# Kernel tuning notes

Measured on AMD Instinct MI355X. Metric: run time of the kernel, lower is better.

The kernel has to match this reference:

```python
import jax, jax.numpy as jnp
import numpy as np

B, C, H = 2, 32, 64  # batch, base channel, bottleneck spatial size
EPS = 1e-5


def _conv(x, w, b, pad):
    # standard NCHW conv, stride 1
    out = jax.lax.conv_general_dilated(x, w, (1, 1), [(pad, pad), (pad, pad)],
                                       dimension_numbers=("NCHW", "OIHW", "NCHW"))
    return out + b[None, :, None, None]


def _inorm(x):
    # InstanceNorm2d, affine=False (torch default)
    m = jnp.mean(x, axis=(2, 3), keepdims=True)
    v = jnp.var(x, axis=(2, 3), keepdims=True)
    return (x - m) * jax.lax.rsqrt(v + EPS)


def _patches3(x):
    # x: (B,C,H,W) -> (B,C,9,H-2,W-2); 3x3 patches, stride 1, VALID
    oh, ow = x.shape[-2] - 2, x.shape[-1] - 2
    return jnp.stack([x[:, :, i:i + oh, j:j + ow] for i in range(3) for j in range(3)], axis=2)


def _pac_kernel(g):
    # gaussian pixel-adaptive kernel (NVlabs/pac, kernel_type='gaussian', normalize_kernel=False)
    # g: (B,Cg,H,W) -> K: (B,9,H,W), K = exp(-0.5*||f_nbr - f_center||^2)
    gp = jnp.pad(g, ((0, 0), (0, 0), (1, 1), (1, 1)))
    p = _patches3(gp)                      # (B,Cg,9,H,W)
    d = p - g[:, :, None]                  # center is offset (1,1) == g itself
    return jnp.exp(-0.5 * jnp.sum(d * d, axis=1))


def _pacconvT(x, g, w, b):
    # PacConvTranspose2d: kernel_size=3, stride=2, padding=1, output_padding=1
    # native impl: zero-upsample, pad (k-1)-p=1 left/top and 1+out_pad=2 right/bottom,
    # then pixel-adaptive conv with weight.permute(1,0,2,3) (no spatial flip, per PAC).
    Bc, Cin, Hh, Ww = x.shape
    z = jnp.zeros((Bc, Cin, 2 * Hh - 1, 2 * Ww - 1), x.dtype).at[:, :, ::2, ::2].set(x)
    z = jnp.pad(z, ((0, 0), (0, 0), (1, 2), (1, 2)))
    p = _patches3(z)                       # (B,Cin,9,2H,2W)
    k = _pac_kernel(g)                     # (B,9,2H,2W)
    wf = jnp.transpose(w, (1, 0, 2, 3)).reshape(w.shape[1], w.shape[0], 9)  # (Cout,Cin,9)
    out = jnp.einsum('bckhw,bkhw,ock->bohw', p, k, wf)
    return out + b[None, :, None, None]


def _w(key, shape, scale):
    return jax.random.normal(key, shape, dtype=jnp.float32) * scale


def setup_inputs():
    key = jax.random.key(0)
    ks = jax.random.split(key, 20)
    return {
        "x": jax.random.normal(ks[0], (B, 8 * C, H, H), jnp.float32),
        "ef_lv2": jax.random.normal(ks[1], (B, 2 * C, 2 * H, 2 * H), jnp.float32),
        "ef_lv1": jax.random.normal(ks[2], (B, C, 4 * H, 4 * H), jnp.float32),
        "W_down": _w(ks[3], (4 * C, 8 * C, 3, 3), (8 * C * 9) ** -0.5),
        "b_down": _w(ks[4], (4 * C,), 0.01),
        "W_mid": _w(ks[5], (4 * C, 4 * C, 1, 1), (4 * C) ** -0.5),
        "b_mid": _w(ks[6], (4 * C,), 0.01),
        "W_adj2": _w(ks[7], (4 * C, 2 * C, 3, 3), 0.002),  # small: keeps gaussian kernel non-degenerate
        "b_adj2": _w(ks[8], (4 * C,), 0.01),
        "W_adj1": _w(ks[9], (2 * C, C, 3, 3), 0.004),
        "b_adj1": _w(ks[10], (2 * C,), 0.01),
        "W16": _w(ks[11], (4 * C, 2 * C, 3, 3), (4 * C * 9) ** -0.5),  # convT layout (Cin,Cout,kh,kw)
        "b16": _w(ks[12], (2 * C,), 0.01),
        "W20": _w(ks[13], (2 * C, C, 3, 3), (2 * C * 9) ** -0.5),
        "b20": _w(ks[14], (C,), 0.01),
        "W24": _w(ks[15], (3, C, 3, 3), (C * 9) ** -0.5),
        "b24": _w(ks[16], (3,), 0.01),
    }


def reference(x, ef_lv2, ef_lv1, W_down, b_down, W_mid, b_mid, W_adj2, b_adj2,
              W_adj1, b_adj1, W16, b16, W20, b20, W24, b24):
    x = _conv(_inorm(x), W_down, b_down, 1)          # layer13: norm + channel-down 8C->4C
    x = _conv(x, W_mid, b_mid, 0) + x                # middle_layer13 1x1 + residual
    g2 = _conv(ef_lv2, W_adj2, b_adj2, 1)            # adjust_ef_lv2 2C->4C
    x = _pacconvT(x, g2, W16, b16)                   # layer16: 4C->2C, x2 spatial
    x = _inorm(x) + x                                # layer17 + residual (twice)
    x = _inorm(x) + x
    g1 = _conv(ef_lv1, W_adj1, b_adj1, 1)            # adjust_ef_lv1 C->2C
    x = _pacconvT(x, g1, W20, b20)                   # layer20: 2C->C, x2 spatial
    x = _inorm(x) + x                                # layer21 + residual (twice)
    x = _inorm(x) + x
    return _conv(x, W24, b24, 1)                     # layer24: C->3
```

## Files before the change

### kernel.cpp

```cpp
#include <hip/hip_runtime.h>

#define EPS 1e-5f

typedef short sh8 __attribute__((ext_vector_type(8)));
typedef float f32x4 __attribute__((ext_vector_type(4)));

__device__ __forceinline__ ushort f2b(float f) {
    unsigned u = __float_as_uint(f);
    u += 0x7fffu + ((u >> 16) & 1u);
    return (ushort)(u >> 16);
}

__device__ __forceinline__ void istat_body(int ch, const float* __restrict__ in,
                                           float* st, int HW)
{
    __shared__ double sh[512];
    const float* p = in + (size_t)ch * HW;
    double s = 0.0, s2 = 0.0;
    for (int i = threadIdx.x * 4; i < HW; i += 1024) {
        float4 v = *(const float4*)(p + i);
        s  += (double)v.x + (double)v.y + (double)v.z + (double)v.w;
        s2 += (double)v.x * v.x + (double)v.y * v.y
            + (double)v.z * v.z + (double)v.w * v.w;
    }
    sh[threadIdx.x] = s; sh[256 + threadIdx.x] = s2;
    __syncthreads();
    for (int o = 128; o > 0; o >>= 1) {
        if ((int)threadIdx.x < o) {
            sh[threadIdx.x]       += sh[threadIdx.x + o];
            sh[256 + threadIdx.x] += sh[256 + threadIdx.x + o];
        }
        __syncthreads();
    }
    if (threadIdx.x == 0) {
        double m = sh[0] / (double)HW;
        double v = sh[256] / (double)HW - m * m;
        st[2 * ch]     = (float)m;
        st[2 * ch + 1] = (float)(v < 0.0 ? 0.0 : v);
    }
}

__device__ __forceinline__ void ipad_body(int bxi, int b,
    const float* __restrict__ in, const float* __restrict__ st,
    ushort* __restrict__ ob, int C, int H, int W, int pad, int n4)
{
    int idx = bxi * 256 + threadIdx.x;
    if (idx >= n4) return;
    int cpp = C >> 2;
    int pp = idx / cpp, c0 = (idx - pp * cpp) * 4;
    int Wp = W + 2 * pad, Hp = H + 2 * pad;
    int yp = pp / Wp, xp = pp - yp * Wp;
    int y = yp - pad, x = xp - pad;
    ushort4 o;
    if (y >= 0 && y < H && x >= 0 && x < W) {
        size_t HW = (size_t)H * W;
        const float* ib = in + (size_t)b * C * HW + (size_t)y * W + x;
        #pragma unroll
        for (int u = 0; u < 4; u++) {
            int chg = b * C + c0 + u;
            float m = st[2 * chg];
            float inv = rsqrtf(st[2 * chg + 1] + EPS);
            float v = ib[(size_t)(c0 + u) * HW];
            ((ushort*)&o)[u] = f2b((v - m) * inv);
        }
    } else { o.x = o.y = o.z = o.w = 0; }
    *(ushort4*)(ob + ((size_t)b * Hp * Wp + pp) * C + c0) = o;
}

__device__ __forceinline__ void pad_body(int bxi, int b,
    const float* __restrict__ in, ushort* __restrict__ ob,
    int C, int H, int W, int pad, int n4)
{
    int idx = bxi * 256 + threadIdx.x;
    if (idx >= n4) return;
    int cpp = C >> 2;
    int pp = idx / cpp, c0 = (idx - pp * cpp) * 4;
    int Wp = W + 2 * pad, Hp = H + 2 * pad;
    int yp = pp / Wp, xp = pp - yp * Wp;
    int y = yp - pad, x = xp - pad;
    ushort4 o;
    if (y >= 0 && y < H && x >= 0 && x < W) {
        const float* ib = in + ((size_t)b * C) * H * W + (size_t)y * W + x;
        size_t HW = (size_t)H * W;
        o.x = f2b(ib[(size_t)(c0    ) * HW]);
        o.y = f2b(ib[(size_t)(c0 + 1) * HW]);
        o.z = f2b(ib[(size_t)(c0 + 2) * HW]);
        o.w = f2b(ib[(size_t)(c0 + 3) * HW]);
    } else { o.x = o.y = o.z = o.w = 0; }
    *(ushort4*)(ob + ((size_t)b * Hp * Wp + pp) * C + c0) = o;
}

__device__ __forceinline__ void wprep_body(int bxi,
    const float* W16, const float* W20, const float* Wd, const float* Wa2,
    const float* Wa1,
    ushort* wT1b, ushort* wT2b, ushort* wbD, ushort* wbA2b, ushort* wbA1b)
{
    int idx = bxi * 256 + threadIdx.x;
    if (idx < 73728) {
        int to = idx / 128, ci = idx - to * 128;
        int t = to / 64, o = to - t * 64;
        wT1b[idx] = f2b(W16[((size_t)ci * 64 + o) * 9 + t]);
        return;
    } idx -= 73728;
    if (idx < 18432) {
        int to = idx / 64, ci = idx - to * 64;
        int t = to / 32, o = to - t * 32;
        wT2b[idx] = f2b(W20[((size_t)ci * 32 + o) * 9 + t]);
        return;
    } idx -= 18432;
    if (idx < 294912) {
        int co = idx / 2304, r = idx - co * 2304;
        int t = r / 256, ci = r - t * 256;
        wbD[idx] = f2b(Wd[((size_t)co * 256 + ci) * 9 + t]);
        return;
    } idx -= 294912;
    if (idx < 73728) {
        int co = idx / 576, r = idx - co * 576;
        int t = r / 64, ci = r - t * 64;
        wbA2b[idx] = f2b(Wa2[((size_t)co * 64 + ci) * 9 + t]);
        return;
    } idx -= 73728;
    if (idx < 18432) {
        int co = idx / 288, r = idx - co * 288;
        int t = r / 32, ci = r - t * 32;
        wbA1b[idx] = f2b(Wa1[((size_t)co * 32 + ci) * 9 + t]);
        return;
    }
}

template<int CI, int TAPS, int KCH, int CPB>
__device__ __forceinline__ void mg2f_body(int bx, int by, int bz,
    const ushort* __restrict__ inb, const ushort* __restrict__ wb,
    const float* __restrict__ bias, float* __restrict__ outp,
    int wshift, int Wp, int NS, size_t SS,
    size_t in_bstride, size_t out_bstride, int HW, ushort* bsm)
{
    constexpr int CPBSH = (CPB == 1) ? 0 : (CPB == 2) ? 1 : 2;
    constexpr int SPR   = TAPS * CPB;
    constexpr int TOT   = TAPS * KCH;
    constexpr int PS    = SPR * 32 + 8;

    int b = bz / NS, sl = bz - b * NS;
    int cilo = sl * (KCH * 32);
    int tid = threadIdx.x;
    int wv = tid >> 6, l = tid & 63;
    int lane16 = l & 15, quad = l >> 4;
    int klane = quad * 8;
    int pb = bx * 128 + wv * 32;
    int nb0 = by * 32;

    int base[2];
    #pragma unroll
    for (int i = 0; i < 2; i++) {
        int pm = pb + i * 16 + lane16;
        if (TAPS == 9) {
            int W = 1 << wshift;
            int y = pm >> wshift, xx = pm & (W - 1);
            base[i] = (y + 1) * Wp + (xx + 1);
        } else base[i] = pm;
    }
    int nn[2];
    nn[0] = nb0 + lane16; nn[1] = nb0 + 16 + lane16;

    const ushort* inbb = inb + (size_t)b * in_bstride + cilo + klane;
    const ushort* wbs  = wb + cilo;
    const ushort* bp0 = bsm + lane16 * PS + klane;
    const ushort* bp1 = bsm + (16 + lane16) * PS + klane;

    f32x4 vz = {0.f, 0.f, 0.f, 0.f};
    f32x4 acc[2][2] = {{vz, vz}, {vz, vz}};
    sh8 A[3][2];

    #define LDA(ss, av) { \
        int r_ = (ss) / SPR; int l_ = (ss) - r_ * SPR; \
        int t_ = l_ >> CPBSH; int ch_ = r_ * CPB + (l_ & (CPB - 1)); \
        int dof_ = 0; \
        if (TAPS == 9) { \
            int dy_ = (t_ * 43) >> 7; \
            int dx_ = t_ - dy_ * 3; \
            dof_ = (dy_ - 1) * Wp + (dx_ - 1); \
        } \
        av[0] = *(const sh8*)(inbb + (size_t)(base[0] + dof_) * CI + (ch_ << 5)); \
        av[1] = *(const sh8*)(inbb + (size_t)(base[1] + dof_) * CI + (ch_ << 5)); \
    }

    LDA(0, A[0])
    if (TOT > 1) LDA(1, A[1])

    #pragma unroll
    for (int r = 0; r < KCH / CPB; r++) {
        if (r) __syncthreads();
        {
            constexpr int elems = 32 * SPR * 4;
            for (int j = tid; j < elems; j += 256) {
                int n  = j / (SPR * 4);
                int rr = j - n * (SPR * 4);
                int kc = rr >> 2, c8 = rr & 3;
                int t_ = kc >> CPBSH, co = kc & (CPB - 1);
                int ch_ = r * CPB + co;
                sh8 v = *(const sh8*)(wbs
                    + ((size_t)(nb0 + n) * TAPS + t_) * CI + (ch_ << 5) + (c8 << 3));
                *(sh8*)(bsm + n * PS + (kc << 5) + (c8 << 3)) = v;
            }
        }
        __syncthreads();
        #pragma unroll
        for (int li = 0; li < SPR; li++) {
            const int s = r * SPR + li;
            if (s + 2 < TOT) LDA(s + 2, A[(s + 2) % 3])
            sh8 b0 = *(const sh8*)(bp0 + (li << 5));
            sh8 b1 = *(const sh8*)(bp1 + (li << 5));
            acc[0][0] = __builtin_amdgcn_mfma_f32_16x16x32_bf16(A[s % 3][0], b0, acc[0][0], 0, 0, 0);
            acc[0][1] = __builtin_amdgcn_mfma_f32_16x16x32_bf16(A[s % 3][0], b1, acc[0][1], 0, 0, 0);
            acc[1][0] = __builtin_amdgcn_mfma_f32_16x16x32_bf16(A[s % 3][1], b0, acc[1][0], 0, 0, 0);
            acc[1][1] = __builtin_amdgcn_mfma_f32_16x16x32_bf16(A[s % 3][1], b1, acc[1][1], 0, 0, 0);
        }
    }
    #undef LDA

    float* ob = outp + (size_t)sl * SS + (size_t)b * out_bstride;
    #pragma unroll
    for (int j = 0; j < 2; j++) {
        float bb = bias ? bias[nn[j]] : 0.f;
        #pragma unroll
        for (int i = 0; i < 2; i++) {
            int p0 = pb + i * 16 + quad * 4;
            *(float4*)(ob + (size_t)nn[j] * HW + p0) =
                make_float4(acc[i][j][0] + bb, acc[i][j][1] + bb,
                            acc[i][j][2] + bb, acc[i][j][3] + bb);
        }
    }
}

__device__ __forceinline__ void pack4_body(int bxi, int zy,
    const float* __restrict__ g, float* __restrict__ part,
    int Cg, int CS, int H, int W, int NS, size_t SS)
{
    int b = zy / NS, sl = zy - b * NS;
    int WC = W >> 2;
    int idx = bxi * 256 + threadIdx.x;
    int y = idx / WC, xc = idx - y * WC;
    int x0 = xc << 2;
    bool lz = (x0 == 0), rz = (x0 + 4 == W);
    float acc[9][4];
    #pragma unroll
    for (int t = 0; t < 9; t++)
        #pragma unroll
        for (int p = 0; p < 4; p++) acc[t][p] = 0.f;

    const float* gb = g + ((size_t)b * Cg + sl * CS) * H * W;
    for (int ci = 0; ci < CS; ci++) {
        const float* gc = gb + (size_t)ci * H * W;
        float e[3][6];
        #pragma unroll
        for (int r = 0; r < 3; r++) {
            int yy = y + r - 1;
            float4 v = make_float4(0.f, 0.f, 0.f, 0.f);
            if (yy >= 0 && yy < H)
                v = *(const float4*)(gc + (size_t)yy * W + x0);
            float lf = __shfl_up(v.w, 1);
            float rt = __shfl_down(v.x, 1);
            e[r][0] = lz ? 0.f : lf;
            e[r][1] = v.x; e[r][2] = v.y; e[r][3] = v.z; e[r][4] = v.w;
            e[r][5] = rz ? 0.f : rt;
        }
        #pragma unroll
        for (int i = 0; i < 3; i++)
            #pragma unroll
            for (int j = 0; j < 3; j++)
                #pragma unroll
                for (int p = 0; p < 4; p++) {
                    float d = e[i][p + j] - e[1][p + 1];
                    acc[i * 3 + j][p] = fmaf(d, d, acc[i * 3 + j][p]);
                }
    }
    size_t HW = (size_t)H * W;
    #pragma unroll
    for (int t = 0; t < 9; t++) {
        float4 o;
        if (NS == 1) {
            o = make_float4(expf(-0.5f * acc[t][0]), expf(-0.5f * acc[t][1]),
                            expf(-0.5f * acc[t][2]), expf(-0.5f * acc[t][3]));
        } else {
            o = make_float4(acc[t][0], acc[t][1], acc[t][2], acc[t][3]);
        }
        *(float4*)(part + (size_t)sl * SS + ((size_t)b * 9 + t) * HW
                   + (size_t)y * W + x0) = o;
    }
}

__device__ __forceinline__ void reduce_body(int bxi,
    const float* __restrict__ part, const float* __restrict__ bias,
    const float* res, float* out, int HW, int Co, int NS, size_t SS)
{
    int i4 = (bxi * 256 + threadIdx.x) * 4;
    float4 a = make_float4(0.f, 0.f, 0.f, 0.f);
    for (int s = 0; s < NS; s++) {
        float4 p = *(const float4*)(part + (size_t)s * SS + i4);
        a.x += p.x; a.y += p.y; a.z += p.z; a.w += p.w;
    }
    int c = (i4 / HW) % Co;
    float bb = bias[c];
    if (res) {
        float4 r = *(const float4*)(res + i4);
        a.x += r.x; a.y += r.y; a.z += r.z; a.w += r.w;
    }
    *(float4*)(out + i4) = make_float4(a.x + bb, a.y + bb, a.z + bb, a.w + bb);
}

__device__ __forceinline__ void expcomb_body(int bxi,
    const float* __restrict__ part, float* __restrict__ K, int NS, size_t SS)
{
    int i4 = (bxi * 256 + threadIdx.x) * 4;
    float4 a = make_float4(0.f, 0.f, 0.f, 0.f);
    for (int s = 0; s < NS; s++) {
        float4 p = *(const float4*)(part + (size_t)s * SS + i4);
        a.x += p.x; a.y += p.y; a.z += p.z; a.w += p.w;
    }
    *(float4*)(K + i4) = make_float4(expf(-0.5f * a.x), expf(-0.5f * a.y),
                                     expf(-0.5f * a.z), expf(-0.5f * a.w));
}

__global__ __launch_bounds__(256) void pro_k(
    const float* x, const float* ef2, const float* ef1,
    const float* W16, const float* W20, const float* Wd, const float* Wa2,
    const float* Wa1,
    ushort* wT1b, ushort* wT2b, ushort* wbD, ushort* wbA2b, ushort* wbA1b,
    float* st0, ushort* padA2b, ushort* padA1b)
{
    int bid = blockIdx.x;
    if (bid < 1872) {
        wprep_body(bid, W16, W20, Wd, Wa2, Wa1, wT1b, wT2b, wbD, wbA2b, wbA1b);
        return;
    } bid -= 1872;
    if (bid < 512) { istat_body(bid, x, st0, 4096); return; } bid -= 512;
    if (bid < 2114) {
        pad_body(bid % 1057, bid / 1057, ef2, padA2b, 64, 128, 128, 1, 270400);
        return;
    } bid -= 2114;
    pad_body(bid % 2081, bid / 2081, ef1, padA1b, 32, 256, 256, 1, 532512);
}

__global__ __launch_bounds__(256) void l1_k(
    const float* x, const float* st0, ushort* padDb,
    const ushort* padA2b, const ushort* wbA2b, const float* ba2, float* g2,
    const ushort* padA1b, const ushort* wbA1b, const float* ba1, float* g1)
{
    __shared__ ushort smem[32 * (9 * 32 + 8)];
    int bid = blockIdx.x;
    if (bid < 2178) {
        ipad_body(bid % 1089, bid / 1089, x, st0, padDb, 256, 64, 64, 1, 278784);
        return;
    } bid -= 2178;
    if (bid < 1024) {
        mg2f_body<64, 9, 2, 1>(bid & 127, (bid >> 7) & 3, bid >> 9,
            padA2b, wbA2b, ba2, g2, 7, 130, 1, (size_t)0,
            (size_t)1081600, (size_t)2097152, 16384, smem);
        return;
    } bid -= 1024;
    mg2f_body<32, 9, 1, 1>(bid & 511, (bid >> 9) & 1, bid >> 10,
        padA1b, wbA1b, ba1, g1, 8, 258, 1, (size_t)0,
        (size_t)2130048, (size_t)4194304, 65536, smem);
}

__global__ __launch_bounds__(256) void l2_k(
    const ushort* padDb, const ushort* wbD, float* Pd,
    const float* g1, float* PK1, const float* g2, float* PK2)
{
    __shared__ ushort smem[32 * (9 * 32 + 8)];
    int bid = blockIdx.x;
    if (bid < 512) {
        pack4_body(bid & 63, bid >> 6, g1, PK1, 64, 16, 256, 256, 4, (size_t)1179648);
        return;
    } bid -= 512;
    if (bid < 256) {
        pack4_body(bid & 15, bid >> 4, g2, PK2, 128, 16, 128, 128, 8, (size_t)294912);
        return;
    } bid -= 256;
    mg2f_body<256, 9, 1, 1>(bid & 31, (bid >> 5) & 3, bid >> 7,
        padDb, wbD, nullptr, Pd, 6, 66, 8, (size_t)1048576,
        (size_t)1115136, (size_t)524288, 4096, smem);
}

__global__ __launch_bounds__(256) void l3_k(
    const float* Pd, const float* bd, float* x1,
    const float* PK1, float* K1, const float* PK2, float* K2)
{
    int bid = blockIdx.x;
    if (bid < 1024) {
        reduce_body(bid, Pd, bd, nullptr, x1, 4096, 128, 8, (size_t)1048576);
        return;
    } bid -= 1024;
    if (bid < 1152) {
        expcomb_body(bid, PK1, K1, 4, (size_t)1179648);
        return;
    } bid -= 1152;
    expcomb_body(bid, PK2, K2, 8, (size_t)294912);
}

__global__ __launch_bounds__(256) void conv1x1f_k(
    const float* __restrict__ x1, const float* __restrict__ Wm,
    const float* __restrict__ bm, ushort* __restrict__ x2b)
{
    __shared__ float wsm[1024];
    int b = blockIdx.z;
    int co0 = blockIdx.y * 8;
    int tid = threadIdx.x;
    for (int j = tid; j < 1024; j += 256) {
        int co = j >> 7, ci = j & 127;
        wsm[j] = Wm[(size_t)(co0 + co) * 128 + ci];
    }
    __syncthreads();
    int px0 = (blockIdx.x * 256 + tid) * 4;
    const float* ib = x1 + (size_t)b * 524288 + px0;
    float acc[8][4];
    #pragma unroll
    for (int j = 0; j < 8; j++)
        #pragma unroll
        for (int p = 0; p < 4; p++) acc[j][p] = 0.f;
    for (int ci = 0; ci < 128; ci++) {
        float4 v = *(const float4*)(ib + (size_t)ci * 4096);
        #pragma unroll
        for (int j = 0; j < 8; j++) {
            float wv = wsm[j * 128 + ci];
            acc[j][0] = fmaf(v.x, wv, acc[j][0]);
            acc[j][1] = fmaf(v.y, wv, acc[j][1]);
            acc[j][2] = fmaf(v.z, wv, acc[j][2]);
            acc[j][3] = fmaf(v.w, wv, acc[j][3]);
        }
    }
    float vals[4][8];
    #pragma unroll
    for (int j = 0; j < 8; j++) {
        float4 r = *(const float4*)(ib + (size_t)(co0 + j) * 4096);
        float bb = bm[co0 + j];
        vals[0][j] = acc[j][0] + r.x + bb;
        vals[1][j] = acc[j][1] + r.y + bb;
        vals[2][j] = acc[j][2] + r.z + bb;
        vals[3][j] = acc[j][3] + r.w + bb;
    }
    #pragma unroll
    for (int p = 0; p < 4; p++) {
        sh8 ov;
        #pragma unroll
        for (int j = 0; j < 8; j++) ((ushort*)&ov)[j] = f2b(vals[p][j]);
        *(sh8*)(x2b + ((size_t)b * 4096 + px0 + p) * 128 + co0) = ov;
    }
}

__global__ __launch_bounds__(256) void istat1_k(const float* __restrict__ in,
                                                float* st, int HW)
{
    istat_body(blockIdx.x, in, st, HW);
}

template<int CI, int TAPS, int KCH, int CPB>
__global__ __launch_bounds__(256) void mg2f_k(
    const ushort* __restrict__ inb, const ushort* __restrict__ wb,
    const float* __restrict__ bias, float* __restrict__ outp,
    int wshift, int Wp, int NS, size_t SS,
    size_t in_bstride, size_t out_bstride, int HW)
{
    constexpr int PS = TAPS * CPB * 32 + 8;
    __shared__ ushort smem[32 * PS];
    mg2f_body<CI, TAPS, KCH, CPB>(blockIdx.x, blockIdx.y, blockIdx.z,
        inb, wb, bias, outp, wshift, Wp, NS, SS, in_bstride, out_bstride, HW, smem);
}

__global__ __launch_bounds__(256) void iapad_k(const float* __restrict__ in,
    const float* __restrict__ st, ushort* __restrict__ ob, int HW, int Co)
{
    int i4 = (blockIdx.x * 256 + threadIdx.x) * 4;
    int ch = i4 / HW;
    int p = i4 - ch * HW;
    int b = ch / Co, c = ch - b * Co;
    float m = st[2 * ch];
    float inv = rsqrtf(st[2 * ch + 1] + EPS);
    float4 v = *(const float4*)(in + i4);
    ushort* op = ob + ((size_t)b * HW + p) * Co + c;
    op[0]              = f2b(v.x + 2.f * (v.x - m) * inv);
    op[(size_t)Co]     = f2b(v.y + 2.f * (v.y - m) * inv);
    op[(size_t)Co * 2] = f2b(v.z + 2.f * (v.z - m) * inv);
    op[(size_t)Co * 3] = f2b(v.w + 2.f * (v.w - m) * inv);
}

template<int NCO>
__global__ __launch_bounds__(256) void conv3x3_d(const float* __restrict__ in,
    const float* __restrict__ w, const float* __restrict__ bias,
    float* __restrict__ outp, const float* __restrict__ st,
    int Ci, int CS, int H, int W, int Co, int NS, size_t SS)
{
    int z = blockIdx.z;
    int b = z / NS, sl = z - b * NS;
    int WC = W >> 2;
    int idx = blockIdx.x * 256 + threadIdx.x;
    int xc = idx % WC, y = idx / WC;
    int x0 = xc << 2;
    bool lz = (x0 == 0), rz = (x0 + 4 == W);
    int co0 = blockIdx.y * NCO;
    float acc[NCO][4];
    #pragma unroll
    for (int j = 0; j < NCO; j++)
        #pragma unroll
        for (int p = 0; p < 4; p++) acc[j][p] = 0.f;

    const float* ib = in + ((size_t)b * Ci + sl * CS) * H * W;
    for (int ci = 0; ci < CS; ci++) {
        const float* ic = ib + (size_t)ci * H * W;
        int cig = sl * CS + ci;
        float sa = 1.f, sb = 0.f;
        if (st) {
            int chg = b * Ci + cig;
            float m = st[2 * chg];
            float inv = rsqrtf(st[2 * chg + 1] + EPS);
            sa = 1.f + 2.f * inv;
            sb = -2.f * m * inv;
        }
        float e[3][6];
        #pragma unroll
        for (int r = 0; r < 3; r++) {
            int yy = y + r - 1;
            float4 v = make_float4(0.f, 0.f, 0.f, 0.f);
            if (yy >= 0 && yy < H) {
                v = *(const float4*)(ic + (size_t)yy * W + x0);
                if (st) {
                    v.x = fmaf(v.x, sa, sb); v.y = fmaf(v.y, sa, sb);
                    v.z = fmaf(v.z, sa, sb); v.w = fmaf(v.w, sa, sb);
                }
            }
            float lf = __shfl_up(v.w, 1);
            float rt = __shfl_down(v.x, 1);
            e[r][0] = lz ? 0.f : lf;
            e[r][1] = v.x; e[r][2] = v.y; e[r][3] = v.z; e[r][4] = v.w;
            e[r][5] = rz ? 0.f : rt;
        }
        #pragma unroll
        for (int j = 0; j < NCO; j++) {
            const float* wj = w + ((size_t)(co0 + j) * Ci + cig) * 9;
            #pragma unroll
            for (int r = 0; r < 3; r++) {
                float w0 = wj[3 * r], w1 = wj[3 * r + 1], w2 = wj[3 * r + 2];
                #pragma unroll
                for (int p = 0; p < 4; p++)
                    acc[j][p] = fmaf(e[r][p], w0,
                                fmaf(e[r][p + 1], w1,
                                fmaf(e[r][p + 2], w2, acc[j][p])));
            }
        }
    }
    size_t HW = (size_t)H * W;
    #pragma unroll
    for (int j = 0; j < NCO; j++) {
        float bb = bias ? bias[co0 + j] : 0.f;
        float4 o = make_float4(acc[j][0] + bb, acc[j][1] + bb,
                               acc[j][2] + bb, acc[j][3] + bb);
        float* op = outp + (size_t)sl * SS
                  + ((size_t)b * Co + co0 + j) * HW + (size_t)y * W + x0;
        *(float4*)op = o;
    }
}

__global__ __launch_bounds__(256) void reduce_k(const float* __restrict__ part,
    const float* __restrict__ bias, const float* res, float* out,
    int HW, int Co, int NS, size_t SS)
{
    reduce_body(blockIdx.x, part, bias, res, out, HW, Co, NS, SS);
}

template<int NCO>
__global__ __launch_bounds__(256) void pacsc_k(const float* __restrict__ Gin,
    const float* __restrict__ K, const float* __restrict__ bias,
    float* __restrict__ out, int Cout, int Hi, int Wi, size_t gstride)
{
    int b = blockIdx.z;
    int H = Hi << 1, W = Wi << 1;
    int HW = H * W, HWi = Hi * Wi, WC = W >> 2;
    int idx = blockIdx.x * 256 + threadIdx.x;
    int half = (H >> 1) * WC;
    int py = (idx >= half) ? 1 : 0;
    int r = idx - py * half;
    int ry = r / WC;
    int y = 2 * ry + py;
    int x0 = (r - ry * WC) << 2;
    int yi = y >> 1, xi0 = x0 >> 1;
    int co0 = blockIdx.y * NCO;
    const float* G  = Gin + (size_t)b * gstride;
    const float* Kb = K + (size_t)b * 9 * HW;
    float* ob = out + (size_t)b * Cout * HW;
    size_t krow = (size_t)y * W + x0;
    bool vok = (xi0 + 2 < Wi);

    if (py == 0) {
        float k4a = Kb[(size_t)4 * HW + krow],     k4b = Kb[(size_t)4 * HW + krow + 2];
        float k3a = Kb[(size_t)3 * HW + krow + 1], k3b = Kb[(size_t)3 * HW + krow + 3];
        float k5a = Kb[(size_t)5 * HW + krow + 1], k5b = Kb[(size_t)5 * HW + krow + 3];
        #pragma unroll
        for (int j = 0; j < NCO; j++) {
            int co = co0 + j;
            size_t rowb = (size_t)yi * Wi + xi0;
            const float* g3 = G + (size_t)(3 * Cout + co) * HWi + rowb;
            const float* g4 = G + (size_t)(4 * Cout + co) * HWi + rowb;
            const float* g5 = G + (size_t)(5 * Cout + co) * HWi + rowb;
            float bb = bias[co];
            float g5b = vok ? g5[2] : 0.f;
            float o0 = fmaf(k4a, g4[0], bb);
            float o1 = fmaf(k3a, g3[0], fmaf(k5a, g5[1], bb));
            float o2 = fmaf(k4b, g4[1], bb);
            float o3 = fmaf(k3b, g3[1], fmaf(k5b, g5b, bb));
            *(float4*)(ob + (size_t)co * HW + krow) = make_float4(o0, o1, o2, o3);
        }
    } else {
        bool yok = (yi + 1 < Hi);
        float k1a = Kb[(size_t)1 * HW + krow],     k1b = Kb[(size_t)1 * HW + krow + 2];
        float k7a = Kb[(size_t)7 * HW + krow],     k7b = Kb[(size_t)7 * HW + krow + 2];
        float k0a = Kb[(size_t)0 * HW + krow + 1], k0b = Kb[(size_t)0 * HW + krow + 3];
        float k2a = Kb[(size_t)2 * HW + krow + 1], k2b = Kb[(size_t)2 * HW + krow + 3];
        float k6a = Kb[(size_t)6 * HW + krow + 1], k6b = Kb[(size_t)6 * HW + krow + 3];
        float k8a = Kb[(size_t)8 * HW + krow + 1], k8b = Kb[(size_t)8 * HW + krow + 3];
        #pragma unroll
        for (int j = 0; j < NCO; j++) {
            int co = co0 + j;
            size_t row0 = (size_t)yi * Wi + xi0;
            size_t row1 = (size_t)(yi + 1) * Wi + xi0;
            const float* g0 = G + (size_t)(0 * Cout + co) * HWi + row0;
            const float* g1 = G + (size_t)(1 * Cout + co) * HWi + row0;
            const float* g2 = G + (size_t)(2 * Cout + co) * HWi + row0;
            const float* g6 = G + (size_t)(6 * Cout + co) * HWi + row1;
            const float* g7 = G + (size_t)(7 * Cout + co) * HWi + row1;
            const float* g8 = G + (size_t)(8 * Cout + co) * HWi + row1;
            float bb = bias[co];
            float g2b = vok ? g2[2] : 0.f;
            float g6a = yok ? g6[0] : 0.f, g6b = yok ? g6[1] : 0.f;
            float g7a = yok ? g7[0] : 0.f, g7b = yok ? g7[1] : 0.f;
            float g8a = yok ? g8[1] : 0.f;
            float g8b = (yok && vok) ? g8[2] : 0.f;
            float o0 = fmaf(k1a, g1[0], fmaf(k7a, g7a, bb));
            float o1 = fmaf(k0a, g0[0], fmaf(k2a, g2[1],
                       fmaf(k6a, g6a, fmaf(k8a, g8a, bb))));
            float o2 = fmaf(k1b, g1[1], fmaf(k7b, g7b, bb));
            float o3 = fmaf(k0b, g0[1], fmaf(k2b, g2b,
                       fmaf(k6b, g6b, fmaf(k8b, g8b, bb))));
            *(float4*)(ob + (size_t)co * HW + krow) = make_float4(o0, o1, o2, o3);
        }
    }
}

extern "C" void kernel_launch(void* const* d_in, const int* in_sizes, int n_in,
                              void* d_out, int out_size, void* d_ws, size_t ws_size,
                              hipStream_t stream)
{
    const float* x   = (const float*)d_in[0];
    const float* ef2 = (const float*)d_in[1];
    const float* ef1 = (const float*)d_in[2];
    const float* Wd  = (const float*)d_in[3];
    const float* bd  = (const float*)d_in[4];
    const float* Wm  = (const float*)d_in[5];
    const float* bm  = (const float*)d_in[6];
    const float* Wa2 = (const float*)d_in[7];
    const float* ba2 = (const float*)d_in[8];
    const float* Wa1 = (const float*)d_in[9];
    const float* ba1 = (const float*)d_in[10];
    const float* W16 = (const float*)d_in[11];
    const float* b16 = (const float*)d_in[12];
    const float* W20 = (const float*)d_in[13];
    const float* b20 = (const float*)d_in[14];
    const float* W24 = (const float*)d_in[15];
    const float* b24 = (const float*)d_in[16];
    float* out = (float*)d_out;

    float* P = (float*)d_ws;
    size_t o = 0;
    auto take = [&](size_t n) { float* p = P + o; o += n; return p; };
    ushort* padDb  = (ushort*)take(1115136);
    ushort* wbD    = (ushort*)take(147456);
    float*  Pd     = take(8388608);
    float*  x1     = take(1048576);
    ushort* x2b    = (ushort*)take(524288);
    ushort* padA2b = (ushort*)take(1081600);
    ushort* wbA2b  = (ushort*)take(36864);
    float*  g2     = take(4194304);
    float*  PK2    = take(2359296);
    float*  K2     = take(294912);
    float*  Gin1   = take(4718592);
    float*  x3     = take(2097152);
    ushort* x3b    = (ushort*)take(1048576);
    ushort* padA1b = (ushort*)take(2130048);
    ushort* wbA1b  = (ushort*)take(9216);
    float*  g1     = take(8388608);
    float*  PK1    = take(4718592);
    float*  K1     = take(1179648);
    float*  Gin2   = take(9437184);
    float*  x5     = take(4194304);
    float*  Pf     = take(1572864);
    ushort* wT1b   = (ushort*)take(36864);
    ushort* wT2b   = (ushort*)take(9216);
    float*  ST     = take(1408);
    float* st0 = ST; float* st3 = ST + 1024; float* st5 = ST + 1280;

    pro_k<<<dim3(8660), dim3(256), 0, stream>>>(
        x, ef2, ef1, W16, W20, Wd, Wa2, Wa1,
        wT1b, wT2b, wbD, wbA2b, wbA1b, st0, padA2b, padA1b);

    l1_k<<<dim3(5250), dim3(256), 0, stream>>>(
        x, st0, padDb, padA2b, wbA2b, ba2, g2, padA1b, wbA1b, ba1, g1);

    l2_k<<<dim3(2816), dim3(256), 0, stream>>>(
        padDb, wbD, Pd, g1, PK1, g2, PK2);

    l3_k<<<dim3(2464), dim3(256), 0, stream>>>(Pd, bd, x1, PK1, K1, PK2, K2);

    conv1x1f_k<<<dim3(4, 16, 2), dim3(256), 0, stream>>>(x1, Wm, bm, x2b);

    mg2f_k<128, 1, 4, 4><<<dim3(32, 18, 2), dim3(256), 0, stream>>>(
        x2b, wT1b, nullptr, Gin1, 0, 0, 1, (size_t)0,
        (size_t)524288, (size_t)2359296, 4096);
    pacsc_k<2><<<dim3(16, 32, 2), dim3(256), 0, stream>>>(
        Gin1, K2, b16, x3, 64, 64, 64, (size_t)2359296);

    istat1_k<<<dim3(128), dim3(256), 0, stream>>>(x3, st3, 16384);
    iapad_k<<<dim3(2048), dim3(256), 0, stream>>>(x3, st3, x3b, 16384, 64);

    mg2f_k<64, 1, 2, 2><<<dim3(128, 9, 2), dim3(256), 0, stream>>>(
        x3b, wT2b, nullptr, Gin2, 0, 0, 1, (size_t)0,
        (size_t)1048576, (size_t)4718592, 16384);
    pacsc_k<2><<<dim3(64, 16, 2), dim3(256), 0, stream>>>(
        Gin2, K1, b20, x5, 32, 128, 128, (size_t)4718592);

    istat1_k<<<dim3(64), dim3(256), 0, stream>>>(x5, st5, 65536);

    conv3x3_d<3><<<dim3(64, 1, 8), dim3(256), 0, stream>>>(
        x5, W24, nullptr, Pf, st5, 32, 8, 256, 256, 3, 4, (size_t)393216);
    reduce_k<<<dim3(384), dim3(256), 0, stream>>>(Pf, b24, nullptr, out, 65536, 3, 4, 393216);
}
```

Measured before the change: 325.3 us.

## Fuse instance-norm statistics into PAC scatter kernels via atomics, drop istat launches

Each pacsc_k block now reduces per-channel sums and sums of squares in double and atomically adds them into a zeroed stats buffer, so the two separate istat1_k passes over x3 and x5 are removed. iapad_k and conv3x3_d derive mean and variance from those raw sums. The MFMA A-operand prefetch depth goes from 2 to 3 stages, and conv1x1f_k is split into twice as many blocks with 4 output channels each. The cost is double-precision atomics and shuffles, and the variance is now computed as E[x²]−mean², which can lose precision when the mean is large.

```diff
diff --git a/kernel.cpp b/kernel.cpp
--- a/kernel.cpp
+++ b/kernel.cpp
@@ -169,7 +169,7 @@
 
     f32x4 vz = {0.f, 0.f, 0.f, 0.f};
     f32x4 acc[2][2] = {{vz, vz}, {vz, vz}};
-    sh8 A[3][2];
+    sh8 A[4][2];
 
     #define LDA(ss, av) { \
         int r_ = (ss) / SPR; int l_ = (ss) - r_ * SPR; \
@@ -186,6 +186,7 @@
 
     LDA(0, A[0])
     if (TOT > 1) LDA(1, A[1])
+    if (TOT > 2) LDA(2, A[2])
 
     #pragma unroll
     for (int r = 0; r < KCH / CPB; r++) {
@@ -207,13 +208,13 @@
         #pragma unroll
         for (int li = 0; li < SPR; li++) {
             const int s = r * SPR + li;
-            if (s + 2 < TOT) LDA(s + 2, A[(s + 2) % 3])
+            if (s + 3 < TOT) LDA(s + 3, A[(s + 3) & 3])
             sh8 b0 = *(const sh8*)(bp0 + (li << 5));
             sh8 b1 = *(const sh8*)(bp1 + (li << 5));
-            acc[0][0] = __builtin_amdgcn_mfma_f32_16x16x32_bf16(A[s % 3][0], b0, acc[0][0], 0, 0, 0);
-            acc[0][1] = __builtin_amdgcn_mfma_f32_16x16x32_bf16(A[s % 3][0], b1, acc[0][1], 0, 0, 0);
-            acc[1][0] = __builtin_amdgcn_mfma_f32_16x16x32_bf16(A[s % 3][1], b0, acc[1][0], 0, 0, 0);
-            acc[1][1] = __builtin_amdgcn_mfma_f32_16x16x32_bf16(A[s % 3][1], b1, acc[1][1], 0, 0, 0);
+            acc[0][0] = __builtin_amdgcn_mfma_f32_16x16x32_bf16(A[s & 3][0], b0, acc[0][0], 0, 0, 0);
+            acc[0][1] = __builtin_amdgcn_mfma_f32_16x16x32_bf16(A[s & 3][0], b1, acc[0][1], 0, 0, 0);
+            acc[1][0] = __builtin_amdgcn_mfma_f32_16x16x32_bf16(A[s & 3][1], b0, acc[1][0], 0, 0, 0);
+            acc[1][1] = __builtin_amdgcn_mfma_f32_16x16x32_bf16(A[s & 3][1], b1, acc[1][1], 0, 0, 0);
         }
     }
     #undef LDA
@@ -384,9 +385,12 @@
 
 __global__ __launch_bounds__(256) void l3_k(
     const float* Pd, const float* bd, float* x1,
-    const float* PK1, float* K1, const float* PK2, float* K2)
+    const float* PK1, float* K1, const float* PK2, float* K2, double* sta)
 {
     int bid = blockIdx.x;
+    if (bid == 0) {
+        for (int t = threadIdx.x; t < 384; t += 256) sta[t] = 0.0;
+    }
     if (bid < 1024) {
         reduce_body(bid, Pd, bd, nullptr, x1, 4096, 128, 8, (size_t)1048576);
         return;
@@ -402,26 +406,26 @@
     const float* __restrict__ x1, const float* __restrict__ Wm,
     const float* __restrict__ bm, ushort* __restrict__ x2b)
 {
-    __shared__ float wsm[1024];
+    __shared__ float wsm[512];
     int b = blockIdx.z;
-    int co0 = blockIdx.y * 8;
+    int co0 = blockIdx.y * 4;
     int tid = threadIdx.x;
-    for (int j = tid; j < 1024; j += 256) {
+    for (int j = tid; j < 512; j += 256) {
         int co = j >> 7, ci = j & 127;
         wsm[j] = Wm[(size_t)(co0 + co) * 128 + ci];
     }
     __syncthreads();
     int px0 = (blockIdx.x * 256 + tid) * 4;
     const float* ib = x1 + (size_t)b * 524288 + px0;
-    float acc[8][4];
-    #pragma unroll
-    for (int j = 0; j < 8; j++)
+    float acc[4][4];
+    #pragma unroll
+    for (int j = 0; j < 4; j++)
         #pragma unroll
         for (int p = 0; p < 4; p++) acc[j][p] = 0.f;
     for (int ci = 0; ci < 128; ci++) {
         float4 v = *(const float4*)(ib + (size_t)ci * 4096);
         #pragma unroll
-        for (int j = 0; j < 8; j++) {
+        for (int j = 0; j < 4; j++) {
             float wv = wsm[j * 128 + ci];
             acc[j][0] = fmaf(v.x, wv, acc[j][0]);
             acc[j][1] = fmaf(v.y, wv, acc[j][1]);
@@ -429,9 +433,9 @@
             acc[j][3] = fmaf(v.w, wv, acc[j][3]);
         }
     }
-    float vals[4][8];
-    #pragma unroll
-    for (int j = 0; j < 8; j++) {
+    float vals[4][4];
+    #pragma unroll
+    for (int j = 0; j < 4; j++) {
         float4 r = *(const float4*)(ib + (size_t)(co0 + j) * 4096);
         float bb = bm[co0 + j];
         vals[0][j] = acc[j][0] + r.x + bb;
@@ -441,17 +445,11 @@
     }
     #pragma unroll
     for (int p = 0; p < 4; p++) {
-        sh8 ov;
-        #pragma unroll
-        for (int j = 0; j < 8; j++) ((ushort*)&ov)[j] = f2b(vals[p][j]);
-        *(sh8*)(x2b + ((size_t)b * 4096 + px0 + p) * 128 + co0) = ov;
-    }
-}
-
-__global__ __launch_bounds__(256) void istat1_k(const float* __restrict__ in,
-                                                float* st, int HW)
-{
-    istat_body(blockIdx.x, in, st, HW);
+        ushort4 ov;
+        ov.x = f2b(vals[p][0]); ov.y = f2b(vals[p][1]);
+        ov.z = f2b(vals[p][2]); ov.w = f2b(vals[p][3]);
+        *(ushort4*)(x2b + ((size_t)b * 4096 + px0 + p) * 128 + co0) = ov;
+    }
 }
 
 template<int CI, int TAPS, int KCH, int CPB>
@@ -468,14 +466,17 @@
 }
 
 __global__ __launch_bounds__(256) void iapad_k(const float* __restrict__ in,
-    const float* __restrict__ st, ushort* __restrict__ ob, int HW, int Co)
+    const double* __restrict__ sta, ushort* __restrict__ ob, int HW, int Co)
 {
     int i4 = (blockIdx.x * 256 + threadIdx.x) * 4;
     int ch = i4 / HW;
     int p = i4 - ch * HW;
     int b = ch / Co, c = ch - b * Co;
-    float m = st[2 * ch];
-    float inv = rsqrtf(st[2 * ch + 1] + EPS);
+    double S = sta[2 * ch], S2 = sta[2 * ch + 1];
+    double md = S / (double)HW;
+    double vr = S2 / (double)HW - md * md;
+    float m = (float)md;
+    float inv = rsqrtf((float)(vr < 0.0 ? 0.0 : vr) + EPS);
     float4 v = *(const float4*)(in + i4);
     ushort* op = ob + ((size_t)b * HW + p) * Co + c;
     op[0]              = f2b(v.x + 2.f * (v.x - m) * inv);
@@ -487,7 +488,7 @@
 template<int NCO>
 __global__ __launch_bounds__(256) void conv3x3_d(const float* __restrict__ in,
     const float* __restrict__ w, const float* __restrict__ bias,
-    float* __restrict__ outp, const float* __restrict__ st,
+    float* __restrict__ outp, const double* __restrict__ sta,
     int Ci, int CS, int H, int W, int Co, int NS, size_t SS)
 {
     int z = blockIdx.z;
@@ -509,12 +510,15 @@
         const float* ic = ib + (size_t)ci * H * W;
         int cig = sl * CS + ci;
         float sa = 1.f, sb = 0.f;
-        if (st) {
+        if (sta) {
             int chg = b * Ci + cig;
-            float m = st[2 * chg];
-            float inv = rsqrtf(st[2 * chg + 1] + EPS);
+            double S = sta[2 * chg], S2 = sta[2 * chg + 1];
+            double n = (double)H * W;
+            double md = S / n;
+            double vr = S2 / n - md * md;
+            float inv = rsqrtf((float)(vr < 0.0 ? 0.0 : vr) + EPS);
             sa = 1.f + 2.f * inv;
-            sb = -2.f * m * inv;
+            sb = -2.f * (float)md * inv;
         }
         float e[3][6];
         #pragma unroll
@@ -523,7 +527,7 @@
             float4 v = make_float4(0.f, 0.f, 0.f, 0.f);
             if (yy >= 0 && yy < H) {
                 v = *(const float4*)(ic + (size_t)yy * W + x0);
-                if (st) {
+                if (sta) {
                     v.x = fmaf(v.x, sa, sb); v.y = fmaf(v.y, sa, sb);
                     v.z = fmaf(v.z, sa, sb); v.w = fmaf(v.w, sa, sb);
                 }
@@ -570,7 +574,8 @@
 template<int NCO>
 __global__ __launch_bounds__(256) void pacsc_k(const float* __restrict__ Gin,
     const float* __restrict__ K, const float* __restrict__ bias,
-    float* __restrict__ out, int Cout, int Hi, int Wi, size_t gstride)
+    float* __restrict__ out, double* __restrict__ sta,
+    int Cout, int Hi, int Wi, size_t gstride)
 {
     int b = blockIdx.z;
     int H = Hi << 1, W = Wi << 1;
@@ -590,6 +595,10 @@
     size_t krow = (size_t)y * W + x0;
     bool vok = (xi0 + 2 < Wi);
 
+    double ts[NCO], ts2[NCO];
+    #pragma unroll
+    for (int j = 0; j < NCO; j++) { ts[j] = 0.0; ts2[j] = 0.0; }
+
     if (py == 0) {
         float k4a = Kb[(size_t)4 * HW + krow],     k4b = Kb[(size_t)4 * HW + krow + 2];
         float k3a = Kb[(size_t)3 * HW + krow + 1], k3b = Kb[(size_t)3 * HW + krow + 3];
@@ -608,6 +617,9 @@
             float o2 = fmaf(k4b, g4[1], bb);
             float o3 = fmaf(k3b, g3[1], fmaf(k5b, g5b, bb));
             *(float4*)(ob + (size_t)co * HW + krow) = make_float4(o0, o1, o2, o3);
+            ts[j]  += (double)o0 + o1 + o2 + o3;
+            ts2[j] += (double)o0 * o0 + (double)o1 * o1
+                    + (double)o2 * o2 + (double)o3 * o3;
         }
     } else {
         bool yok = (yi + 1 < Hi);
@@ -641,7 +653,31 @@
             float o3 = fmaf(k0b, g0[1], fmaf(k2b, g2b,
                        fmaf(k6b, g6b, fmaf(k8b, g8b, bb))));
             *(float4*)(ob + (size_t)co * HW + krow) = make_float4(o0, o1, o2, o3);
-        }
+            ts[j]  += (double)o0 + o1 + o2 + o3;
+            ts2[j] += (double)o0 * o0 + (double)o1 * o1
+                    + (double)o2 * o2 + (double)o3 * o3;
+        }
+    }
+
+    __shared__ double sred[8];
+    int l = threadIdx.x & 63, wv = threadIdx.x >> 6;
+    #pragma unroll
+    for (int j = 0; j < NCO; j++) {
+        double s = ts[j], s2 = ts2[j];
+        for (int off = 32; off > 0; off >>= 1) {
+            s  += __shfl_down(s, off);
+            s2 += __shfl_down(s2, off);
+        }
+        if (l == 0) { sred[wv] = s; sred[4 + wv] = s2; }
+        __syncthreads();
+        if (threadIdx.x == 0) {
+            double S  = sred[0] + sred[1] + sred[2] + sred[3];
+            double S2 = sred[4] + sred[5] + sred[6] + sred[7];
+            int co = co0 + j;
+            atomicAdd(&sta[(size_t)(b * Cout + co) * 2],     S);
+            atomicAdd(&sta[(size_t)(b * Cout + co) * 2 + 1], S2);
+        }
+        __syncthreads();
     }
 }
 
@@ -694,8 +730,9 @@
     float*  Pf     = take(1572864);
     ushort* wT1b   = (ushort*)take(36864);
     ushort* wT2b   = (ushort*)take(9216);
-    float*  ST     = take(1408);
-    float* st0 = ST; float* st3 = ST + 1024; float* st5 = ST + 1280;
+    float*  ST     = take(1024);
+    double* STA    = (double*)take(768);
+    float* st0 = ST;
 
     pro_k<<<dim3(8660), dim3(256), 0, stream>>>(
         x, ef2, ef1, W16, W20, Wd, Wa2, Wa1,
@@ -707,28 +744,25 @@
     l2_k<<<dim3(2816), dim3(256), 0, stream>>>(
         padDb, wbD, Pd, g1, PK1, g2, PK2);
 
-    l3_k<<<dim3(2464), dim3(256), 0, stream>>>(Pd, bd, x1, PK1, K1, PK2, K2);
-
-    conv1x1f_k<<<dim3(4, 16, 2), dim3(256), 0, stream>>>(x1, Wm, bm, x2b);
+    l3_k<<<dim3(2464), dim3(256), 0, stream>>>(Pd, bd, x1, PK1, K1, PK2, K2, STA);
+
+    conv1x1f_k<<<dim3(4, 32, 2), dim3(256), 0, stream>>>(x1, Wm, bm, x2b);
 
     mg2f_k<128, 1, 4, 4><<<dim3(32, 18, 2), dim3(256), 0, stream>>>(
         x2b, wT1b, nullptr, Gin1, 0, 0, 1, (size_t)0,
         (size_t)524288, (size_t)2359296, 4096);
     pacsc_k<2><<<dim3(16, 32, 2), dim3(256), 0, stream>>>(
-        Gin1, K2, b16, x3, 64, 64, 64, (size_t)2359296);
-
-    istat1_k<<<dim3(128), dim3(256), 0, stream>>>(x3, st3, 16384);
-    iapad_k<<<dim3(2048), dim3(256), 0, stream>>>(x3, st3, x3b, 16384, 64);
+        Gin1, K2, b16, x3, STA, 64, 64, 64, (size_t)2359296);
+
+    iapad_k<<<dim3(2048), dim3(256), 0, stream>>>(x3, STA, x3b, 16384, 64);
 
     mg2f_k<64, 1, 2, 2><<<dim3(128, 9, 2), dim3(256), 0, stream>>>(
         x3b, wT2b, nullptr, Gin2, 0, 0, 1, (size_t)0,
         (size_t)1048576, (size_t)4718592, 16384);
     pacsc_k<2><<<dim3(64, 16, 2), dim3(256), 0, stream>>>(
-        Gin2, K1, b20, x5, 32, 128, 128, (size_t)4718592);
-
-    istat1_k<<<dim3(64), dim3(256), 0, stream>>>(x5, st5, 65536);
+        Gin2, K1, b20, x5, STA + 256, 32, 128, 128, (size_t)4718592);
 
     conv3x3_d<3><<<dim3(64, 1, 8), dim3(256), 0, stream>>>(
-        x5, W24, nullptr, Pf, st5, 32, 8, 256, 256, 3, 4, (size_t)393216);
+        x5, W24, nullptr, Pf, STA + 256, 32, 8, 256, 256, 3, 4, (size_t)393216);
     reduce_k<<<dim3(384), dim3(256), 0, stream>>>(Pf, b24, nullptr, out, 65536, 3, 4, 393216);
 }
```

New measurement: 313.7 us. 3.6% less time.
